# Kernel optimization log

Measured on AMD Instinct MI355X. Metric: run time of the kernel, lower is better.

Reference implementation:

```python
import jax, jax.numpy as jnp
import numpy as np

N_HEAD = 16

def setup_inputs() -> dict:
    key = jax.random.key(0)
    k1, k2, k3 = jax.random.split(key, 3)
    B, T, C = 2, 2048, 2048
    x = jax.random.normal(k1, (B, T, C), dtype=jnp.float32)
    # torch Linear weights are [out, in]; init with small scale for stability
    w_attn = jax.random.normal(k2, (3 * C, C), dtype=jnp.float32) * 0.02
    b_attn = jnp.zeros((3 * C,), dtype=jnp.float32)
    w_proj = jax.random.normal(k3, (C, C), dtype=jnp.float32) * 0.02
    b_proj = jnp.zeros((C,), dtype=jnp.float32)
    return {"x": x, "w_attn": w_attn, "b_attn": b_attn, "w_proj": w_proj, "b_proj": b_proj}

def reference(x, w_attn, b_attn, w_proj, b_proj):
    B, T, C = x.shape
    nh = N_HEAD
    hs = C // nh
    # fused QKV projection (torch Linear: x @ W^T + b)
    qkv = x @ w_attn.T + b_attn                      # [B, T, 3C]
    q, k, v = jnp.split(qkv, 3, axis=2)
    # [B, nh, T, hs]
    q = q.reshape(B, T, nh, hs).transpose(0, 2, 1, 3)
    k = k.reshape(B, T, nh, hs).transpose(0, 2, 1, 3)
    v = v.reshape(B, T, nh, hs).transpose(0, 2, 1, 3)
    # causal scaled dot-product attention
    scale = 1.0 / jnp.sqrt(jnp.asarray(hs, dtype=x.dtype))
    logits = jnp.einsum("bhqd,bhkd->bhqk", q, k) * scale  # [B, nh, T, T]
    causal = jnp.tril(jnp.ones((T, T), dtype=bool))
    logits = jnp.where(causal, logits, jnp.finfo(logits.dtype).min)
    attn = jax.nn.softmax(logits, axis=-1)
    y = jnp.einsum("bhqk,bhkd->bhqd", attn, v)       # [B, nh, T, hs]
    y = y.transpose(0, 2, 1, 3).reshape(B, T, C)
    # output projection (resid_dropout is identity in eval / p=0)
    y = y @ w_proj.T + b_proj
    return y
```

## Files before the change

### kernel.cpp

```cpp
#include <hip/hip_runtime.h>
#include <stdint.h>

typedef __bf16 bf16_t;
typedef __bf16 bf16x8 __attribute__((ext_vector_type(8)));
typedef float f32x4 __attribute__((ext_vector_type(4)));
typedef unsigned short us16x8 __attribute__((ext_vector_type(8)));

#define MFMA16(a, b, c) __builtin_amdgcn_mfma_f32_16x16x32_bf16(a, b, c, 0, 0, 0)
#define BAR() __builtin_amdgcn_s_barrier()
#define PRIO1() __builtin_amdgcn_s_setprio(1)
#define PRIO0() __builtin_amdgcn_s_setprio(0)
#define LGKM0()                                        \
  do {                                                 \
    asm volatile("s_waitcnt lgkmcnt(0)" ::: "memory"); \
    __builtin_amdgcn_sched_barrier(0);                 \
  } while (0)
#define VMCNT(n)                                          \
  do {                                                    \
    asm volatile("s_waitcnt vmcnt(" #n ")" ::: "memory"); \
    __builtin_amdgcn_sched_barrier(0);                    \
  } while (0)

__device__ __forceinline__ void stage16(const bf16_t* g, bf16_t* l) {
  __builtin_amdgcn_global_load_lds((__attribute__((address_space(1))) void*)g,
                                   (__attribute__((address_space(3))) void*)l, 16, 0, 0);
}

__global__ __launch_bounds__(256) void cvt_f32_to_bf16(const float* __restrict__ in,
                                                       bf16_t* __restrict__ out, int n8) {
  int i = blockIdx.x * 256 + threadIdx.x;
  if (i >= n8) return;
  const f32x4* p = (const f32x4*)(in + (size_t)i * 8);
  f32x4 a = p[0], b = p[1];
  bf16x8 o;
  o[0] = (bf16_t)a[0]; o[1] = (bf16_t)a[1]; o[2] = (bf16_t)a[2]; o[3] = (bf16_t)a[3];
  o[4] = (bf16_t)b[0]; o[5] = (bf16_t)b[1]; o[6] = (bf16_t)b[2]; o[7] = (bf16_t)b[3];
  *(bf16x8*)(out + (size_t)i * 8) = o;
}

template <int OUT_BF16>
__global__ __launch_bounds__(256, 3) void gemm_tb3(const bf16_t* __restrict__ A,
                                                   const bf16_t* __restrict__ B,
                                                   const float* __restrict__ bias,
                                                   void* __restrict__ Cout,
                                                   int M, int N, int K) {
  __shared__ bf16_t SA[3 * 128 * 32];
  __shared__ bf16_t SB[3 * 128 * 32];
  const int tid = threadIdx.x;
  const int l = tid & 63, w = tid >> 6;
  const int l15 = l & 15, l4 = l >> 4;
  const int wm = w >> 1, wn = w & 1;
  const int nbm = M >> 7;
  const int nwg = gridDim.x;
  const int bid = blockIdx.x;
  const int wg = (bid & 7) * (nwg >> 3) + (bid >> 3);
  const int bn = wg / nbm, bm = wg % nbm;

  const int r0 = tid >> 2;
  const int sc = (((tid & 3) ^ ((r0 >> 1) & 3)) << 3);
  const bf16_t* gA = A + (size_t)(bm * 128 + r0) * K + sc;
  const bf16_t* gB = B + (size_t)(bn * 128 + r0) * K + sc;
  const size_t rowK64 = (size_t)64 * K;

  const int swz = (l4 ^ ((l15 >> 1) & 3)) << 3;
  int aoff[4], boff[4];
#pragma unroll
  for (int i = 0; i < 4; ++i) {
    aoff[i] = (wm * 64 + i * 16 + l15) * 32 + swz;
    boff[i] = (wn * 64 + i * 16 + l15) * 32 + swz;
  }

  f32x4 acc[4][4] = {};
  const int nk = K >> 5;

  auto STAGE = [&](int t2, int buf) {
    const size_t ko = (size_t)t2 * 32;
    stage16(gA + ko, SA + buf * 4096 + tid * 8);
    stage16(gA + rowK64 + ko, SA + buf * 4096 + 2048 + tid * 8);
    stage16(gB + ko, SB + buf * 4096 + tid * 8);
    stage16(gB + rowK64 + ko, SB + buf * 4096 + 2048 + tid * 8);
  };

  auto TILE = [&](int t, int bufR, int bufS) {
    const int t2 = (t + 2 < nk) ? t + 2 : nk - 1;
    STAGE(t2, bufS);
    bf16x8 aR[4], bR[4];
#pragma unroll
    for (int i = 0; i < 4; ++i) {
      aR[i] = *(const bf16x8*)(SA + bufR * 4096 + aoff[i]);
      bR[i] = *(const bf16x8*)(SB + bufR * 4096 + boff[i]);
    }
    VMCNT(4);
    BAR();
    LGKM0();
    PRIO1();
#pragma unroll
    for (int mi = 0; mi < 4; ++mi)
#pragma unroll
      for (int ni = 0; ni < 4; ++ni)
        acc[mi][ni] = MFMA16(aR[mi], bR[ni], acc[mi][ni]);
    PRIO0();
    BAR();
  };

  STAGE(0, 0);
  STAGE(1, 1);
  VMCNT(4);
  BAR();

  for (int t = 0; t < nk - 1; t += 3) {
    TILE(t, 0, 2);
    TILE(t + 1, 1, 0);
    TILE(t + 2, 2, 1);
  }
  TILE(nk - 1, 0, 2);
  VMCNT(0);

  const int rbase = bm * 128 + wm * 64 + (l4 << 2);
  const int cbase = bn * 128 + wn * 64 + l15;
#pragma unroll
  for (int ni = 0; ni < 4; ++ni) {
    float bv = bias[cbase + ni * 16];
#pragma unroll
    for (int mi = 0; mi < 4; ++mi)
#pragma unroll
      for (int r = 0; r < 4; ++r) {
        float v = acc[mi][ni][r] + bv;
        size_t off = (size_t)(rbase + mi * 16 + r) * N + (cbase + ni * 16);
        if (OUT_BF16) ((bf16_t*)Cout)[off] = (bf16_t)v;
        else ((float*)Cout)[off] = v;
      }
  }
}

__global__ __launch_bounds__(256, 2) void attn_fwd(const bf16_t* __restrict__ qkv,
                                                   bf16_t* __restrict__ att) {
  __shared__ bf16_t Kt[64 * 128];
  __shared__ bf16_t Vt[128 * 64];
  __shared__ bf16_t Pw[4][16 * 64];

  int bid = blockIdx.x;
  int pair = bid >> 5, bh = bid & 31;
  int h = bh & 15, b = bh >> 4;
  int tid = threadIdx.x;
  int l = tid & 63, w = tid >> 6;
  int l15 = l & 15, l4 = l >> 4, l7 = l & 7;
  const size_t LD = 6144;
  const bf16_t* base = qkv + (size_t)b * 2048 * LD;

#pragma unroll 1
  for (int phase = 0; phase < 2; ++phase) {
    int qt = phase ? 31 - pair : pair;
    int q0 = qt << 6;
    int wq0 = q0 + w * 16;

    bf16x8 qf[4];
#pragma unroll
    for (int kk = 0; kk < 4; ++kk)
      qf[kk] = *(const bf16x8*)(base + (size_t)(wq0 + l15) * LD + h * 128 + kk * 32 + l4 * 8);

    f32x4 acc[8] = {};
    float mrow[4], lrow[4];
#pragma unroll
    for (int r = 0; r < 4; ++r) { mrow[r] = -1e30f; lrow[r] = 0.f; }

    int nkt = qt + 1;
    for (int kt = 0; kt < nkt; ++kt) {
      int kb = kt << 6;
      const bf16_t* vg = base + (size_t)kb * LD + 4096 + h * 128;
      us16x8 va[2], vb[2];
#pragma unroll
      for (int p = 0; p < 2; ++p) {
        int g = p * 256 + tid;
        int kv = (g >> 4) << 1;
        int d0 = (g & 15) << 3;
        va[p] = *(const us16x8*)(vg + (size_t)kv * LD + d0);
        vb[p] = *(const us16x8*)(vg + (size_t)(kv + 1) * LD + d0);
      }
      const bf16_t* kg = base + (size_t)kb * LD + 2048 + h * 128;
#pragma unroll
      for (int i = 0; i < 4; ++i) {
        int e = i * 256 + tid;
        int row = e >> 4, blk = e & 15;
        int src = (blk ^ (row & 7)) << 3;
        stage16(kg + (size_t)row * LD + src, Kt + e * 8);
      }
#pragma unroll
      for (int p = 0; p < 2; ++p) {
        int g = p * 256 + tid;
        int kv = (g >> 4) << 1;
        int d0 = (g & 15) << 3;
        int k8 = kv >> 3, kr = kv & 7;
#pragma unroll
        for (int j = 0; j < 8; ++j) {
          int d = d0 + j;
          int swz = k8 ^ ((d ^ (d >> 3)) & 7);
          unsigned pack = (unsigned)va[p][j] | ((unsigned)vb[p][j] << 16);
          *(unsigned*)(&Vt[d * 64 + swz * 8 + kr]) = pack;
        }
      }
      __syncthreads();

      {
        f32x4 s[4] = {};
        __builtin_amdgcn_s_setprio(1);
#pragma unroll
        for (int kk = 0; kk < 4; ++kk) {
          int blk = (kk * 4 + l4) ^ l7;
#pragma unroll
          for (int n = 0; n < 4; ++n) {
            bf16x8 kf = *(const bf16x8*)(Kt + (n * 16 + l15) * 128 + blk * 8);
            s[n] = MFMA16(qf[kk], kf, s[n]);
          }
        }
        __builtin_amdgcn_s_setprio(0);

        const float sc = 0.08838834764831845f;
        bool needMask = (kb + 63) > wq0;
        float scf[4];
#pragma unroll
        for (int r = 0; r < 4; ++r) {
          int q = wq0 + (l4 << 2) + r;
#pragma unroll
          for (int n = 0; n < 4; ++n) {
            float v = s[n][r] * sc;
            if (needMask && (kb + n * 16 + l15) > q) v = -1e30f;
            s[n][r] = v;
          }
          float mx = fmaxf(fmaxf(s[0][r], s[1][r]), fmaxf(s[2][r], s[3][r]));
          mx = fmaxf(mx, __shfl_xor(mx, 1));
          mx = fmaxf(mx, __shfl_xor(mx, 2));
          mx = fmaxf(mx, __shfl_xor(mx, 4));
          mx = fmaxf(mx, __shfl_xor(mx, 8));
          float mn = fmaxf(mrow[r], mx);
          float sf = __expf(mrow[r] - mn);
          mrow[r] = mn;
          scf[r] = sf;
          float rs = 0.f;
#pragma unroll
          for (int n = 0; n < 4; ++n) {
            float pv = __expf(s[n][r] - mn);
            s[n][r] = pv;
            rs += pv;
          }
          rs += __shfl_xor(rs, 1);
          rs += __shfl_xor(rs, 2);
          rs += __shfl_xor(rs, 4);
          rs += __shfl_xor(rs, 8);
          lrow[r] = lrow[r] * sf + rs;
        }
#pragma unroll
        for (int nd = 0; nd < 8; ++nd)
#pragma unroll
          for (int r = 0; r < 4; ++r)
            acc[nd][r] *= scf[r];
#pragma unroll
        for (int n = 0; n < 4; ++n) {
          int cb8 = n * 2 + (l15 >> 3);
#pragma unroll
          for (int r = 0; r < 4; ++r) {
            int row = (l4 << 2) + r;
            Pw[w][row * 64 + ((cb8 ^ (row & 7)) << 3) + l7] = (bf16_t)s[n][r];
          }
        }
        __builtin_amdgcn_s_setprio(1);
#pragma unroll
        for (int kk2 = 0; kk2 < 2; ++kk2) {
          bf16x8 pa = *(const bf16x8*)(&Pw[w][l15 * 64 + (((kk2 * 4 + l4) ^ l7) << 3)]);
#pragma unroll
          for (int nd = 0; nd < 8; ++nd) {
            int d = nd * 16 + l15;
            int swz = (kk2 * 4 + l4) ^ ((d ^ (d >> 3)) & 7);
            bf16x8 bv = *(const bf16x8*)(&Vt[d * 64 + swz * 8]);
            acc[nd] = MFMA16(pa, bv, acc[nd]);
          }
        }
        __builtin_amdgcn_s_setprio(0);
      }
      __syncthreads();
    }

#pragma unroll
    for (int r = 0; r < 4; ++r) {
      float inv = 1.0f / lrow[r];
      size_t ro = (size_t)(b * 2048 + wq0 + (l4 << 2) + r) * 2048 + h * 128;
#pragma unroll
      for (int nd = 0; nd < 8; ++nd)
        att[ro + nd * 16 + l15] = (bf16_t)(acc[nd][r] * inv);
    }
  }
}

extern "C" void kernel_launch(void* const* d_in, const int* in_sizes, int n_in,
                              void* d_out, int out_size, void* d_ws, size_t ws_size,
                              hipStream_t stream) {
  (void)in_sizes; (void)n_in; (void)out_size; (void)ws_size;
  const float* x = (const float*)d_in[0];
  const float* w_attn = (const float*)d_in[1];
  const float* b_attn = (const float*)d_in[2];
  const float* w_proj = (const float*)d_in[3];
  const float* b_proj = (const float*)d_in[4];
  float* out = (float*)d_out;

  char* ws = (char*)d_ws;
  bf16_t* xb  = (bf16_t*)(ws);
  bf16_t* wab = (bf16_t*)(ws + 16777216);
  bf16_t* wpb = (bf16_t*)(ws + 41943040);
  bf16_t* qkv = (bf16_t*)(ws + 50331648);
  bf16_t* att = xb;

  cvt_f32_to_bf16<<<4096, 256, 0, stream>>>(x, xb, 1048576);
  cvt_f32_to_bf16<<<6144, 256, 0, stream>>>(w_attn, wab, 1572864);
  cvt_f32_to_bf16<<<2048, 256, 0, stream>>>(w_proj, wpb, 524288);

  gemm_tb3<1><<<1536, 256, 0, stream>>>(xb, wab, b_attn, qkv, 4096, 6144, 2048);

  attn_fwd<<<512, 256, 0, stream>>>(qkv, att);

  gemm_tb3<0><<<512, 256, 0, stream>>>(att, wpb, b_proj, out, 4096, 2048, 2048);
}
```

Before: 299.1 us.

## Replace GEMM with 256x128 persistent tiles and quarter-split MFMA/load interleaving

The 128x128 triple-buffered GEMM is replaced by a 256x128-tile, double-buffered kernel with a persistent grid-stride loop over tiles (512 blocks) and an XCD-aware tile mapping. Each K-step is split into four MFMA quarters, with LDS reads and global-to-LDS staging interleaved between barriers. The aim is more arithmetic per LDS byte and better overlap of loads with MFMA work. In exchange it uses more accumulator registers, drops to occupancy 2, and adds more barriers per K-step.

Result: no change. 304.8 us (+1.9%).

```diff
diff --git a/kernel.cpp b/kernel.cpp
--- a/kernel.cpp
+++ b/kernel.cpp
@@ -39,97 +39,144 @@
 }
 
 template <int OUT_BF16>
-__global__ __launch_bounds__(256, 3) void gemm_tb3(const bf16_t* __restrict__ A,
-                                                   const bf16_t* __restrict__ B,
-                                                   const float* __restrict__ bias,
-                                                   void* __restrict__ Cout,
-                                                   int M, int N, int K) {
-  __shared__ bf16_t SA[3 * 128 * 32];
-  __shared__ bf16_t SB[3 * 128 * 32];
+__global__ __launch_bounds__(256, 2) void gemm_q4(const bf16_t* __restrict__ A,
+                                                  const bf16_t* __restrict__ B,
+                                                  const float* __restrict__ bias,
+                                                  void* __restrict__ Cout,
+                                                  int M, int N, int K) {
+  __shared__ bf16_t SA[2 * 256 * 32];
+  __shared__ bf16_t SB[2 * 128 * 32];
   const int tid = threadIdx.x;
   const int l = tid & 63, w = tid >> 6;
   const int l15 = l & 15, l4 = l >> 4;
   const int wm = w >> 1, wn = w & 1;
-  const int nbm = M >> 7;
-  const int nwg = gridDim.x;
-  const int bid = blockIdx.x;
-  const int wg = (bid & 7) * (nwg >> 3) + (bid >> 3);
-  const int bn = wg / nbm, bm = wg % nbm;
+  const int nbn = N >> 7;
+  const int nbm = M >> 8;
+  const int total = nbm * nbn;
+  const int bnpc = nbn >> 3;
 
   const int r0 = tid >> 2;
-  const int sc = (((tid & 3) ^ ((r0 >> 1) & 3)) << 3);
-  const bf16_t* gA = A + (size_t)(bm * 128 + r0) * K + sc;
-  const bf16_t* gB = B + (size_t)(bn * 128 + r0) * K + sc;
-  const size_t rowK64 = (size_t)64 * K;
+  const int scol = (((tid & 3) ^ ((r0 >> 1) & 3)) << 3);
+  const size_t K64 = (size_t)64 * K;
 
   const int swz = (l4 ^ ((l15 >> 1) & 3)) << 3;
-  int aoff[4], boff[4];
-#pragma unroll
-  for (int i = 0; i < 4; ++i) {
-    aoff[i] = (wm * 64 + i * 16 + l15) * 32 + swz;
-    boff[i] = (wn * 64 + i * 16 + l15) * 32 + swz;
-  }
-
-  f32x4 acc[4][4] = {};
+  int aoff[8], boff[4];
+#pragma unroll
+  for (int i = 0; i < 8; ++i) aoff[i] = (wm * 128 + i * 16 + l15) * 32 + swz;
+#pragma unroll
+  for (int i = 0; i < 4; ++i) boff[i] = (wn * 64 + i * 16 + l15) * 32 + swz;
+
   const int nk = K >> 5;
 
-  auto STAGE = [&](int t2, int buf) {
-    const size_t ko = (size_t)t2 * 32;
-    stage16(gA + ko, SA + buf * 4096 + tid * 8);
-    stage16(gA + rowK64 + ko, SA + buf * 4096 + 2048 + tid * 8);
-    stage16(gB + ko, SB + buf * 4096 + tid * 8);
-    stage16(gB + rowK64 + ko, SB + buf * 4096 + 2048 + tid * 8);
-  };
-
-  auto TILE = [&](int t, int bufR, int bufS) {
-    const int t2 = (t + 2 < nk) ? t + 2 : nk - 1;
-    STAGE(t2, bufS);
-    bf16x8 aR[4], bR[4];
-#pragma unroll
-    for (int i = 0; i < 4; ++i) {
-      aR[i] = *(const bf16x8*)(SA + bufR * 4096 + aoff[i]);
-      bR[i] = *(const bf16x8*)(SB + bufR * 4096 + boff[i]);
+  for (int wk = blockIdx.x; wk < total; wk += gridDim.x) {
+    const int c = wk & 7, rr = wk >> 3;
+    const int bm = rr / bnpc;
+    const int bn = c * bnpc + rr % bnpc;
+
+    const bf16_t* gA = A + (size_t)(bm * 256 + r0) * K + scol;
+    const bf16_t* gB = B + (size_t)(bn * 128 + r0) * K + scol;
+
+    f32x4 acc[8][4] = {};
+
+    auto STA = [&](int t, int buf) {
+      const size_t ko = (size_t)t * 32;
+      stage16(gA + ko, SA + buf * 8192 + tid * 8);
+      stage16(gA + K64 + ko, SA + buf * 8192 + 2048 + tid * 8);
+      stage16(gA + 2 * K64 + ko, SA + buf * 8192 + 4096 + tid * 8);
+      stage16(gA + 3 * K64 + ko, SA + buf * 8192 + 6144 + tid * 8);
+    };
+    auto STB = [&](int t, int buf) {
+      const size_t ko = (size_t)t * 32;
+      stage16(gB + ko, SB + buf * 4096 + tid * 8);
+      stage16(gB + K64 + ko, SB + buf * 4096 + 2048 + tid * 8);
+    };
+
+    auto TILE = [&](int t, int cur) {
+      const int t2 = (t + 2 < nk) ? t + 2 : nk - 1;
+      const bf16_t* SAb = SA + cur * 8192;
+      const bf16_t* SBb = SB + cur * 4096;
+      bf16x8 aR[4], bLo[2], bHi[2];
+#pragma unroll
+      for (int i = 0; i < 4; ++i) aR[i] = *(const bf16x8*)(SAb + aoff[i]);
+      bLo[0] = *(const bf16x8*)(SBb + boff[0]);
+      bLo[1] = *(const bf16x8*)(SBb + boff[1]);
+      BAR();
+      LGKM0();
+      PRIO1();
+#pragma unroll
+      for (int mi = 0; mi < 4; ++mi) {
+        acc[mi][0] = MFMA16(aR[mi], bLo[0], acc[mi][0]);
+        acc[mi][1] = MFMA16(aR[mi], bLo[1], acc[mi][1]);
+      }
+      PRIO0();
+      BAR();
+      bHi[0] = *(const bf16x8*)(SBb + boff[2]);
+      bHi[1] = *(const bf16x8*)(SBb + boff[3]);
+      BAR();
+      LGKM0();
+      PRIO1();
+#pragma unroll
+      for (int mi = 0; mi < 4; ++mi) {
+        acc[mi][2] = MFMA16(aR[mi], bHi[0], acc[mi][2]);
+        acc[mi][3] = MFMA16(aR[mi], bHi[1], acc[mi][3]);
+      }
+      PRIO0();
+      BAR();
+#pragma unroll
+      for (int i = 0; i < 4; ++i) aR[i] = *(const bf16x8*)(SAb + aoff[4 + i]);
+      STB(t2, cur);
+      BAR();
+      LGKM0();
+      PRIO1();
+#pragma unroll
+      for (int mi = 0; mi < 4; ++mi) {
+        acc[4 + mi][2] = MFMA16(aR[mi], bHi[0], acc[4 + mi][2]);
+        acc[4 + mi][3] = MFMA16(aR[mi], bHi[1], acc[4 + mi][3]);
+      }
+      PRIO0();
+      BAR();
+      STA(t2, cur);
+      VMCNT(6);
+      BAR();
+      PRIO1();
+#pragma unroll
+      for (int mi = 0; mi < 4; ++mi) {
+        acc[4 + mi][0] = MFMA16(aR[mi], bLo[0], acc[4 + mi][0]);
+        acc[4 + mi][1] = MFMA16(aR[mi], bLo[1], acc[4 + mi][1]);
+      }
+      PRIO0();
+      BAR();
+    };
+
+    STA(0, 0);
+    STB(0, 0);
+    STA(1, 1);
+    STB(1, 1);
+    VMCNT(6);
+    BAR();
+
+#pragma unroll 1
+    for (int t = 0; t < nk; t += 2) {
+      TILE(t, 0);
+      TILE(t + 1, 1);
     }
-    VMCNT(4);
-    BAR();
-    LGKM0();
-    PRIO1();
-#pragma unroll
-    for (int mi = 0; mi < 4; ++mi)
-#pragma unroll
-      for (int ni = 0; ni < 4; ++ni)
-        acc[mi][ni] = MFMA16(aR[mi], bR[ni], acc[mi][ni]);
-    PRIO0();
-    BAR();
-  };
-
-  STAGE(0, 0);
-  STAGE(1, 1);
-  VMCNT(4);
-  BAR();
-
-  for (int t = 0; t < nk - 1; t += 3) {
-    TILE(t, 0, 2);
-    TILE(t + 1, 1, 0);
-    TILE(t + 2, 2, 1);
-  }
-  TILE(nk - 1, 0, 2);
-  VMCNT(0);
-
-  const int rbase = bm * 128 + wm * 64 + (l4 << 2);
-  const int cbase = bn * 128 + wn * 64 + l15;
-#pragma unroll
-  for (int ni = 0; ni < 4; ++ni) {
-    float bv = bias[cbase + ni * 16];
-#pragma unroll
-    for (int mi = 0; mi < 4; ++mi)
-#pragma unroll
-      for (int r = 0; r < 4; ++r) {
-        float v = acc[mi][ni][r] + bv;
-        size_t off = (size_t)(rbase + mi * 16 + r) * N + (cbase + ni * 16);
-        if (OUT_BF16) ((bf16_t*)Cout)[off] = (bf16_t)v;
-        else ((float*)Cout)[off] = v;
-      }
+    VMCNT(0);
+
+    const int rbase = bm * 256 + wm * 128 + (l4 << 2);
+    const int cbase = bn * 128 + wn * 64 + l15;
+#pragma unroll
+    for (int ni = 0; ni < 4; ++ni) {
+      float bv = bias[cbase + ni * 16];
+#pragma unroll
+      for (int mi = 0; mi < 8; ++mi)
+#pragma unroll
+        for (int rx = 0; rx < 4; ++rx) {
+          float v = acc[mi][ni][rx] + bv;
+          size_t off = (size_t)(rbase + mi * 16 + rx) * N + (cbase + ni * 16);
+          if (OUT_BF16) ((bf16_t*)Cout)[off] = (bf16_t)v;
+          else ((float*)Cout)[off] = v;
+        }
+    }
   }
 }
 
@@ -313,9 +360,9 @@
   cvt_f32_to_bf16<<<6144, 256, 0, stream>>>(w_attn, wab, 1572864);
   cvt_f32_to_bf16<<<2048, 256, 0, stream>>>(w_proj, wpb, 524288);
 
-  gemm_tb3<1><<<1536, 256, 0, stream>>>(xb, wab, b_attn, qkv, 4096, 6144, 2048);
+  gemm_q4<1><<<512, 256, 0, stream>>>(xb, wab, b_attn, qkv, 4096, 6144, 2048);
 
   attn_fwd<<<512, 256, 0, stream>>>(qkv, att);
 
-  gemm_tb3<0><<<512, 256, 0, stream>>>(att, wpb, b_proj, out, 4096, 2048, 2048);
-}
+  gemm_q4<0><<<512, 256, 0, stream>>>(att, wpb, b_proj, out, 4096, 2048, 2048);
+}
```
